# Kernel tuning notes

Measured on AMD Instinct MI355X. Metric: run time of the kernel, lower is better.

Reference implementation:

```python
import jax, jax.numpy as jnp
import numpy as np

N_LAYERS, H, D, DFF, V = 6, 16, 1024, 4096, 512
B, S = 4, 2048
DK = D // H
EPS = 1e-6
NEG = -1000000000.0


def _pe_table(max_len, d):
    pos = np.arange(max_len, dtype=np.float32)[:, None]
    div = 1.0 / (10000.0 ** (np.arange(0, d, 2, dtype=np.float32) / d))
    pe = np.zeros((max_len, d), dtype=np.float32)
    pe[:, 0::2] = np.sin(pos * div)
    pe[:, 1::2] = np.cos(pos * div)
    return jnp.asarray(pe[None])  # [1, max_len, d]


def setup_inputs() -> dict:
    key = jax.random.key(0)
    ks = jax.random.split(key, 20)
    f = lambda k, shp: (jax.random.normal(k, shp, dtype=jnp.float32) * 0.02)
    inp = {
        "tgt": jax.random.randint(ks[0], (B, S), 0, V, dtype=jnp.int64),
        "tgt_mask": jnp.tril(jnp.ones((S, S), dtype=jnp.int32))[None],  # [1,S,S] causal
        "emb": f(ks[1], (V, D)),
        "pe": _pe_table(S, D),
        "Wq": f(ks[2], (N_LAYERS, H, D, DK)), "bq": f(ks[3], (N_LAYERS, H, DK)),
        "Wk": f(ks[4], (N_LAYERS, H, D, DK)), "bk": f(ks[5], (N_LAYERS, H, DK)),
        "Wv": f(ks[6], (N_LAYERS, H, D, DK)), "bv": f(ks[7], (N_LAYERS, H, DK)),
        "Wo": f(ks[8], (N_LAYERS, D, D)), "bo": f(ks[9], (N_LAYERS, D)),
        "W1": f(ks[10], (N_LAYERS, D, DFF)), "b1": f(ks[11], (N_LAYERS, DFF)),
        "W2": f(ks[12], (N_LAYERS, DFF, D)), "b2": f(ks[13], (N_LAYERS, D)),
        "ln1_a": jnp.ones((N_LAYERS, D)), "ln1_b": jnp.zeros((N_LAYERS, D)),
        "ln2_a": jnp.ones((N_LAYERS, D)), "ln2_b": jnp.zeros((N_LAYERS, D)),
        "lnf_a": jnp.ones((D,)), "lnf_b": jnp.zeros((D,)),
    }
    return inp


def _ln(x, a, b):
    # torch: a*(x-mean)/(std+eps)+b with unbiased std
    m = x.mean(-1, keepdims=True)
    var = ((x - m) ** 2).sum(-1, keepdims=True) / (x.shape[-1] - 1)
    return a * (x - m) / (jnp.sqrt(var) + EPS) + b


def reference(tgt, tgt_mask, emb, pe, Wq, bq, Wk, bk, Wv, bv, Wo, bo,
              W1, b1, W2, b2, ln1_a, ln1_b, ln2_a, ln2_b, lnf_a, lnf_b):
    d = emb.shape[1]
    s = tgt.shape[1]
    x = emb[tgt] * jnp.sqrt(jnp.float32(d)) + pe[:, :s]  # [B,S,D]
    dk = Wq.shape[-1]
    scale = jnp.sqrt(jnp.float32(dk))

    def layer(x, p):
        wq, bq_, wk, bk_, wv, bv_, wo, bo_, w1, b1_, w2, b2_, a1, g1, a2, g2 = p
        h = _ln(x, a1, g1)
        q = jnp.einsum('bsd,hdk->bhsk', h, wq) + bq_[:, None, :]
        k = jnp.einsum('bsd,hdk->bhsk', h, wk) + bk_[:, None, :]
        v = jnp.einsum('bsd,hdk->bhsk', h, wv) + bv_[:, None, :]
        sc = jnp.einsum('bhsk,bhtk->bhst', q, k) / scale
        sc = jnp.where(tgt_mask[:, None] == 0, jnp.float32(NEG), sc)
        att = jax.nn.softmax(sc, axis=-1)
        o = jnp.einsum('bhst,bhtk->bhsk', att, v)
        o = o.transpose(0, 2, 1, 3).reshape(x.shape)  # concat heads (head order)
        x = x + (o @ wo + bo_)
        h2 = _ln(x, a2, g2)
        x = x + (jnp.maximum(h2 @ w1 + b1_, 0.0) @ w2 + b2_)
        return x, None

    x, _ = jax.lax.scan(layer, x, (Wq, bq, Wk, bk, Wv, bv, Wo, bo,
                                   W1, b1, W2, b2, ln1_a, ln1_b, ln2_a, ln2_b))
    return _ln(x, lnf_a, lnf_b)
```

## Files before the change

### kernel.cpp

```cpp
#include <hip/hip_runtime.h>

typedef __bf16 bf16;
typedef float f32x4 __attribute__((ext_vector_type(4)));
typedef __bf16 bf16x8 __attribute__((ext_vector_type(8)));
typedef __bf16 bf16x4 __attribute__((ext_vector_type(4)));
typedef __bf16 bf16x2 __attribute__((ext_vector_type(2)));

#define NL 6
#define NH 16
#define DM 1024
#define DFF 4096
#define SEQ 2048
#define NB 4
#define NTOK (NB*SEQ)

__device__ __forceinline__ void gload16(const void* g, void* l) {
  __builtin_amdgcn_global_load_lds((const __attribute__((address_space(1))) void*)g,
                                   (__attribute__((address_space(3))) void*)l, 16, 0, 0);
}

__global__ __launch_bounds__(256) void repack_t(const float* __restrict__ src,
                                                bf16* __restrict__ out, int K, int N) {
  const int l = blockIdx.z;
  const int d0 = blockIdx.x * 32, n0 = blockIdx.y * 32;
  __shared__ float t[32][33];
  const int tx = threadIdx.x & 31, ty = threadIdx.x >> 5;
  const float* s = src + (size_t)l * K * N;
  #pragma unroll
  for (int j = 0; j < 4; ++j)
    t[ty*4 + j][tx] = s[(size_t)(d0 + ty*4 + j) * N + n0 + tx];
  __syncthreads();
  bf16* o = out + (size_t)l * N * K;
  #pragma unroll
  for (int j = 0; j < 4; ++j)
    o[(size_t)(n0 + ty*4 + j) * K + d0 + tx] = (bf16)t[tx][ty*4 + j];
}

__global__ __launch_bounds__(256) void repack_qkv(const float* __restrict__ Wq,
                                                  const float* __restrict__ Wk,
                                                  const float* __restrict__ Wv,
                                                  bf16* __restrict__ out) {
  const int l = blockIdx.z;
  const int d0 = blockIdx.x * 32, n0 = blockIdx.y * 32;
  __shared__ float t[32][33];
  const int tx = threadIdx.x & 31, ty = threadIdx.x >> 5;
  const int which = n0 >> 10, h = (n0 & 1023) >> 6, kh0 = n0 & 63;
  const float* W = (which == 0) ? Wq : (which == 1 ? Wk : Wv);
  const float* s = W + ((size_t)(l*NH + h) * DM) * 64 + kh0;
  #pragma unroll
  for (int j = 0; j < 4; ++j)
    t[ty*4 + j][tx] = s[(size_t)(d0 + ty*4 + j) * 64 + tx];
  __syncthreads();
  bf16* o = out + (size_t)l * 3072 * DM + (size_t)n0 * DM + d0;
  #pragma unroll
  for (int j = 0; j < 4; ++j)
    o[(size_t)(ty*4 + j) * DM + tx] = (bf16)t[tx][ty*4 + j];
}

__global__ __launch_bounds__(256) void repack_b(const float* __restrict__ bq,
                                                const float* __restrict__ bk,
                                                const float* __restrict__ bv,
                                                float* __restrict__ out) {
  const int i = blockIdx.x * 256 + threadIdx.x;
  if (i >= NL * 3072) return;
  const int l = i / 3072, n = i % 3072;
  const int which = n >> 10, h = (n >> 6) & 15, kh = n & 63;
  const float* b = (which == 0) ? bq : (which == 1 ? bk : bv);
  out[i] = b[(l*NH + h) * 64 + kh];
}

__global__ __launch_bounds__(256) void embed_k(const int* __restrict__ tgt,
                                               const float* __restrict__ emb,
                                               const float* __restrict__ pe,
                                               float* __restrict__ x) {
  const int i = blockIdx.x;
  const int spos = i & (SEQ - 1);
  const int tok = tgt[i];
  const int tid = threadIdx.x;
  float4 e = ((const float4*)(emb + (size_t)tok * DM))[tid];
  float4 p = ((const float4*)(pe + (size_t)spos * DM))[tid];
  float4 r; r.x = e.x*32.f + p.x; r.y = e.y*32.f + p.y; r.z = e.z*32.f + p.z; r.w = e.w*32.f + p.w;
  ((float4*)(x + (size_t)i * DM))[tid] = r;
}

template<bool OB>
__global__ __launch_bounds__(256) void ln_k(const float* __restrict__ x,
                                            const float* __restrict__ a,
                                            const float* __restrict__ bsh,
                                            bf16* __restrict__ ob, float* __restrict__ of) {
  __shared__ float red[8];
  const int row = blockIdx.x, tid = threadIdx.x;
  const float4 v = ((const float4*)(x + (size_t)row * DM))[tid];
  float s = v.x + v.y + v.z + v.w;
  #pragma unroll
  for (int off = 32; off > 0; off >>= 1) s += __shfl_down(s, off);
  if ((tid & 63) == 0) red[tid >> 6] = s;
  __syncthreads();
  const float mean = (red[0] + red[1] + red[2] + red[3]) * (1.f / 1024.f);
  const float d0 = v.x - mean, d1 = v.y - mean, d2 = v.z - mean, d3 = v.w - mean;
  float ss = d0*d0 + d1*d1 + d2*d2 + d3*d3;
  #pragma unroll
  for (int off = 32; off > 0; off >>= 1) ss += __shfl_down(ss, off);
  if ((tid & 63) == 0) red[4 + (tid >> 6)] = ss;
  __syncthreads();
  const float var = (red[4] + red[5] + red[6] + red[7]) * (1.f / 1023.f);
  const float inv = 1.f / (sqrtf(var) + 1e-6f);
  const float4 av = ((const float4*)a)[tid];
  const float4 bv = ((const float4*)bsh)[tid];
  const float r0 = av.x * d0 * inv + bv.x;
  const float r1 = av.y * d1 * inv + bv.y;
  const float r2 = av.z * d2 * inv + bv.z;
  const float r3 = av.w * d3 * inv + bv.w;
  if (OB) {
    bf16x4 w; w[0] = (bf16)r0; w[1] = (bf16)r1; w[2] = (bf16)r2; w[3] = (bf16)r3;
    ((bf16x4*)(ob + (size_t)row * DM))[tid] = w;
  } else {
    float4 w; w.x = r0; w.y = r1; w.z = r2; w.w = r3;
    ((float4*)(of + (size_t)row * DM))[tid] = w;
  }
}

#define BARRIER() asm volatile("s_barrier" ::: "memory")
#define VMW(n)    asm volatile("s_waitcnt vmcnt(" #n ")" ::: "memory")

template<int EPI>
__global__ __launch_bounds__(512, 1) void gemm8(const bf16* __restrict__ A,
                                                const bf16* __restrict__ B,
                                                const float* __restrict__ bias,
                                                float* __restrict__ xres,
                                                bf16* __restrict__ outb,
                                                bf16* __restrict__ vtb,
                                                int K, int ldc) {
  constexpr bool SW = (EPI == 1) || (EPI == 2);
  __shared__ __align__(16) char lds[131072];
  const int tid = threadIdx.x;
  const int m0 = blockIdx.x * 256, n0 = blockIdx.y * 256;
  const int wid = tid >> 6, lane = tid & 63;
  const int wm = wid >> 2, wn = wid & 3;
  const int fr = lane & 15, fq = lane >> 4;
  const int fl16 = (fq * 16 + fr) * 16;
  const int s0 = tid, s1 = tid + 512;
  const int r0 = ((s0 >> 7) << 4) | (s0 & 15), c0 = (((s0 >> 6) & 1) << 2) | ((s0 >> 4) & 3);
  const int r1 = ((s1 >> 7) << 4) | (s1 & 15), c1 = (((s1 >> 6) & 1) << 2) | ((s1 >> 4) & 3);
  const bf16* Ap0 = A + (size_t)(m0 + r0) * K + c0 * 8;
  const bf16* Ap1 = A + (size_t)(m0 + r1) * K + c1 * 8;
  const bf16* Bp0 = B + (size_t)(n0 + r0) * K + c0 * 8;
  const bf16* Bp1 = B + (size_t)(n0 + r1) * K + c1 * 8;
  const size_t rskip = (size_t)128 * K;
  const int aRd = wm * 16384;
  const int bRd = 32768 + (wn >> 1) * 16384;
  const int bN = (wn & 1) * 4;

  f32x4 acc[8][4] = {};
  bf16x8 af8[8][2], bfr[4][2];

#define ST_A(d, h, kt) { \
  gload16(Ap0 + (size_t)(h) * rskip + (kt), lds + (d)*65536 + (h)*16384 + s0*16); \
  gload16(Ap1 + (size_t)(h) * rskip + (kt), lds + (d)*65536 + (h)*16384 + s1*16); }
#define ST_B(d, h, kt) { \
  gload16(Bp0 + (size_t)(h) * rskip + (kt), lds + (d)*65536 + 32768 + (h)*16384 + s0*16); \
  gload16(Bp1 + (size_t)(h) * rskip + (kt), lds + (d)*65536 + 32768 + (h)*16384 + s1*16); }
#define LD_A(d, mb) { _Pragma("unroll") for (int m_ = 0; m_ < 4; ++m_) \
    _Pragma("unroll") for (int ks_ = 0; ks_ < 2; ++ks_) \
      af8[(mb) + m_][ks_] = *(const bf16x8*)(lds + (d)*65536 + aRd + ((mb) + m_)*2048 + ks_*1024 + fl16); }
#define LD_B(d, nb) { _Pragma("unroll") for (int n_ = 0; n_ < 2; ++n_) \
    _Pragma("unroll") for (int ks_ = 0; ks_ < 2; ++ks_) \
      bfr[(nb) + n_][ks_] = *(const bf16x8*)(lds + (d)*65536 + bRd + (bN + (nb) + n_)*2048 + ks_*1024 + fl16); }
#define MFMA_Q(mb, nb) { __builtin_amdgcn_s_setprio(1); \
  _Pragma("unroll") for (int m_ = 0; m_ < 4; ++m_) \
  _Pragma("unroll") for (int n_ = 0; n_ < 2; ++n_) \
  _Pragma("unroll") for (int ks_ = 0; ks_ < 2; ++ks_) \
    acc[(mb) + m_][(nb) + n_] = SW ? \
      __builtin_amdgcn_mfma_f32_16x16x32_bf16( \
        bfr[(nb) + n_][ks_], af8[(mb) + m_][ks_], acc[(mb) + m_][(nb) + n_], 0, 0, 0) : \
      __builtin_amdgcn_mfma_f32_16x16x32_bf16( \
        af8[(mb) + m_][ks_], bfr[(nb) + n_][ks_], acc[(mb) + m_][(nb) + n_], 0, 0, 0); \
  __builtin_amdgcn_s_setprio(0); }

  ST_A(0, 0, 0); ST_A(0, 1, 0);
  ST_B(0, 0, 0); ST_B(0, 1, 0);
  ST_A(1, 0, 64); ST_A(1, 1, 64);
  VMW(4);
  BARRIER();

  const int niter = K >> 7;
  for (int it = 0; it < niter; ++it) {
    const int ktB1 = (2 * it + 1) << 6;
    const int ktE2 = (2 * it + 2) << 6;
    const int ktO3 = (2 * it + 3) << 6;
    const bool more = (it + 1 < niter);
    LD_A(0, 0); LD_B(0, 0);
    ST_B(1, 0, ktB1);
    BARRIER(); MFMA_Q(0, 0); BARRIER();
    LD_A(0, 4);
    ST_B(1, 1, ktB1);
    BARRIER(); MFMA_Q(4, 0); BARRIER();
    LD_B(0, 2);
    if (more) ST_A(0, 0, ktE2);
    BARRIER(); MFMA_Q(4, 2); BARRIER();
    if (more) { ST_A(0, 1, ktE2); VMW(4); } else { VMW(0); }
    BARRIER(); MFMA_Q(0, 2); BARRIER();
    LD_A(1, 0); LD_B(1, 0);
    if (more) ST_B(0, 0, ktE2);
    BARRIER(); MFMA_Q(0, 0); BARRIER();
    LD_A(1, 4);
    if (more) ST_B(0, 1, ktE2);
    BARRIER(); MFMA_Q(4, 0); BARRIER();
    LD_B(1, 2);
    if (more) ST_A(1, 0, ktO3);
    BARRIER(); MFMA_Q(4, 2); BARRIER();
    if (more) { ST_A(1, 1, ktO3); VMW(4); }
    BARRIER(); MFMA_Q(0, 2); BARRIER();
  }
#undef ST_A
#undef ST_B
#undef LD_A
#undef LD_B
#undef MFMA_Q

  #pragma unroll
  for (int m = 0; m < 8; ++m) {
    #pragma unroll
    for (int n = 0; n < 4; ++n) {
      if constexpr (SW) {
        const int row = m0 + wm * 128 + m * 16 + fr;
        const int colb = n0 + wn * 64 + n * 16 + fq * 4;
        const float4 b4 = *(const float4*)(bias + colb);
        if constexpr (EPI == 2) {
          bf16x4 w;
          w[0] = (bf16)fmaxf(acc[m][n][0] + b4.x, 0.f);
          w[1] = (bf16)fmaxf(acc[m][n][1] + b4.y, 0.f);
          w[2] = (bf16)fmaxf(acc[m][n][2] + b4.z, 0.f);
          w[3] = (bf16)fmaxf(acc[m][n][3] + b4.w, 0.f);
          *(bf16x4*)(outb + (size_t)row * ldc + colb) = w;
        } else {
          float4* p = (float4*)(xres + (size_t)row * ldc + colb);
          float4 c = *p;
          c.x += acc[m][n][0] + b4.x;
          c.y += acc[m][n][1] + b4.y;
          c.z += acc[m][n][2] + b4.z;
          c.w += acc[m][n][3] + b4.w;
          *p = c;
        }
      } else {
        const int row = m0 + wm * 128 + m * 16 + fq * 4;
        const int col = n0 + wn * 64 + n * 16 + fr;
        const float bc = bias[col];
        #pragma unroll
        for (int j = 0; j < 4; ++j) {
          const float v = acc[m][n][j] + bc;
          outb[(size_t)(row + j) * ldc + col] = (bf16)v;
        }
      }
    }
  }
}

template<int EPI>
__global__ __launch_bounds__(512, 1) void gemm8n(const bf16* __restrict__ A,
                                                 const bf16* __restrict__ B,
                                                 const float* __restrict__ bias,
                                                 float* __restrict__ xres,
                                                 bf16* __restrict__ outb,
                                                 bf16* __restrict__ vtb,
                                                 int K, int ldc) {
  constexpr bool SW = (EPI == 1) || (EPI == 2);
  __shared__ __align__(16) char lds[131072];
  const int tid = threadIdx.x;
  const int m0 = blockIdx.x * 128, n0 = blockIdx.y * 256;
  const int wid = tid >> 6, lane = tid & 63;
  const int wm = wid >> 2, wn = wid & 3;
  const int fr = lane & 15, fq = lane >> 4;
  const int fl16 = (fq * 16 + fr) * 16;
  const int s0 = tid, s1 = tid + 512;
  const int r0 = ((s0 >> 7) << 4) | (s0 & 15), c0 = (((s0 >> 6) & 1) << 2) | ((s0 >> 4) & 3);
  const int r1 = ((s1 >> 7) << 4) | (s1 & 15), c1 = (((s1 >> 6) & 1) << 2) | ((s1 >> 4) & 3);
  const bf16* Ap0 = A + (size_t)(m0 + r0) * K + c0 * 8;
  const bf16* Ap1 = A + (size_t)(m0 + r1) * K + c1 * 8;
  const bf16* Bp0 = B + (size_t)(n0 + r0) * K + c0 * 8;
  const bf16* Bp1 = B + (size_t)(n0 + r1) * K + c1 * 8;
  const size_t rskipB = (size_t)128 * K;
  const int aRd = wm * 8192;
  const int bRd = wn * 8192;

  f32x4 acc[4][4] = {};
  bf16x8 af[4][2], bfr[4][2];

#define ST_An(d, kt) { \
  gload16(Ap0 + (kt), lds + (d)*16384 + s0*16); \
  gload16(Ap1 + (kt), lds + (d)*16384 + s1*16); }
#define ST_Bn(j, h, kt) { \
  gload16(Bp0 + (size_t)(h) * rskipB + (kt), lds + 32768 + (j)*32768 + (h)*16384 + s0*16); \
  gload16(Bp1 + (size_t)(h) * rskipB + (kt), lds + 32768 + (j)*32768 + (h)*16384 + s1*16); }
#define LD_An(d) { _Pragma("unroll") for (int m_ = 0; m_ < 4; ++m_) \
    _Pragma("unroll") for (int ks_ = 0; ks_ < 2; ++ks_) \
      af[m_][ks_] = *(const bf16x8*)(lds + (d)*16384 + aRd + m_*2048 + ks_*1024 + fl16); }
#define LD_Bn(j, nb) { _Pragma("unroll") for (int n_ = 0; n_ < 2; ++n_) \
    _Pragma("unroll") for (int ks_ = 0; ks_ < 2; ++ks_) \
      bfr[(nb) + n_][ks_] = *(const bf16x8*)(lds + 32768 + (j)*32768 + bRd + ((nb) + n_)*2048 + ks_*1024 + fl16); }
#define MFMA_H(nb) { __builtin_amdgcn_s_setprio(1); \
  _Pragma("unroll") for (int m_ = 0; m_ < 4; ++m_) \
  _Pragma("unroll") for (int n_ = 0; n_ < 2; ++n_) \
  _Pragma("unroll") for (int ks_ = 0; ks_ < 2; ++ks_) \
    acc[m_][(nb) + n_] = SW ? \
      __builtin_amdgcn_mfma_f32_16x16x32_bf16( \
        bfr[(nb) + n_][ks_], af[m_][ks_], acc[m_][(nb) + n_], 0, 0, 0) : \
      __builtin_amdgcn_mfma_f32_16x16x32_bf16( \
        af[m_][ks_], bfr[(nb) + n_][ks_], acc[m_][(nb) + n_], 0, 0, 0); \
  __builtin_amdgcn_s_setprio(0); }

  ST_An(0, 0);
  ST_Bn(0, 0, 0); ST_Bn(0, 1, 0);
  ST_An(1, 64);
  ST_Bn(1, 0, 64); ST_Bn(1, 1, 64);
  VMW(0);
  BARRIER();

  const int nt = K >> 6;
  int j = 0;
  for (int t = 0; t < nt; ++t) {
    const int d = t & 1;
    const int j2 = (j + 2 >= 3) ? (j - 1) : (j + 2);
    const bool more = (t + 2 < nt);
    const int kt2 = (t + 2) << 6;
    LD_An(d); LD_Bn(j, 0);
    if (more) { ST_Bn(j2, 0, kt2); ST_Bn(j2, 1, kt2); }
    BARRIER(); MFMA_H(0); BARRIER();
    LD_Bn(j, 2);
    if (more) { ST_An(d, kt2); VMW(6); } else { VMW(0); }
    BARRIER(); MFMA_H(2); BARRIER();
    j = (j + 1 >= 3) ? 0 : (j + 1);
  }
#undef ST_An
#undef ST_Bn
#undef LD_An
#undef LD_Bn
#undef MFMA_H

  #pragma unroll
  for (int m = 0; m < 4; ++m) {
    #pragma unroll
    for (int n = 0; n < 4; ++n) {
      if constexpr (SW) {
        const int row = m0 + wm * 64 + m * 16 + fr;
        const int colb = n0 + wn * 64 + n * 16 + fq * 4;
        const float4 b4 = *(const float4*)(bias + colb);
        if constexpr (EPI == 2) {
          bf16x4 w;
          w[0] = (bf16)fmaxf(acc[m][n][0] + b4.x, 0.f);
          w[1] = (bf16)fmaxf(acc[m][n][1] + b4.y, 0.f);
          w[2] = (bf16)fmaxf(acc[m][n][2] + b4.z, 0.f);
          w[3] = (bf16)fmaxf(acc[m][n][3] + b4.w, 0.f);
          *(bf16x4*)(outb + (size_t)row * ldc + colb) = w;
        } else {
          float4* p = (float4*)(xres + (size_t)row * ldc + colb);
          float4 c = *p;
          c.x += acc[m][n][0] + b4.x;
          c.y += acc[m][n][1] + b4.y;
          c.z += acc[m][n][2] + b4.z;
          c.w += acc[m][n][3] + b4.w;
          *p = c;
        }
      } else {
        const int row = m0 + wm * 64 + m * 16 + fq * 4;
        const int col = n0 + wn * 64 + n * 16 + fr;
        const float bc = bias[col];
        if constexpr (EPI == 3) {
          if (col >= 2048) {
            const int hh = (col - 2048) >> 6, dkk = col & 63;
            const int bb = row >> 11, tt = row & 2047;
            bf16x4 w;
            #pragma unroll
            for (int jj = 0; jj < 4; ++jj) w[jj] = (bf16)(acc[m][n][jj] + bc);
            *(bf16x4*)(vtb + ((((size_t)bb*NH + hh)*64 + dkk)*SEQ + tt)) = w;
            continue;
          }
        }
        #pragma unroll
        for (int jj = 0; jj < 4; ++jj) {
          float v = acc[m][n][jj] + bc;
          if constexpr (EPI == 3) {
            if (col < 1024) v *= 0.125f;
          }
          outb[(size_t)(row + jj) * ldc + col] = (bf16)v;
        }
      }
    }
  }
}

__global__ __launch_bounds__(256) void attn5_k(const bf16* __restrict__ qk,
                                               const bf16* __restrict__ vt,
                                               bf16* __restrict__ o) {
  __shared__ __align__(16) bf16 Ks[2][64 * 64];
  __shared__ __align__(16) bf16 Vs[2][64 * 64];
  __shared__ __align__(16) bf16 Ps[4][16 * 64];
  const int flat = blockIdx.y * 16 + blockIdx.x;
  const int xcd = flat & 7, slot = flat >> 3;
  const int bh = xcd * 8 + (slot >> 4);
  const int pairi = slot & 15;
  const int b = bh >> 4, h = bh & 15;
  const int tid = threadIdx.x;
  const int wave = tid >> 6, lane = tid & 63;
  const int fr = lane & 15, fq = lane >> 4;
  const bf16* Qg = qk + (size_t)b * SEQ * 2048 + h * 64;
  const bf16* Kg = Qg + 1024;
  const bf16* Vtg = vt + (size_t)bh * 64 * SEQ;
  char* Pw = (char*)&Ps[wave][0];
  const int fr7 = fr & 7;

  const int sl0 = tid, sl1 = tid + 256;
  const int sr0 = sl0 >> 3, sm0 = sl0 & 7, sg0 = (sm0 ^ (sr0 & 7)) * 8;
  const int sr1 = sl1 >> 3, sm1 = sl1 & 7, sg1 = (sm1 ^ (sr1 & 7)) * 8;

#define STAGE_KV(db, t0_) { \
    gload16(Kg + (size_t)((t0_) + sr0) * 2048 + sg0, (char*)Ks + (db)*8192 + sl0*16); \
    gload16(Vtg + (size_t)sr0 * SEQ + (t0_) + sg0,   (char*)Vs + (db)*8192 + sl0*16); \
    gload16(Kg + (size_t)((t0_) + sr1) * 2048 + sg1, (char*)Ks + (db)*8192 + sl1*16); \
    gload16(Vtg + (size_t)sr1 * SEQ + (t0_) + sg1,   (char*)Vs + (db)*8192 + sl1*16); }

#define COMPUTE(q0w_, qrow_, qf0_, qf1_, oacc_, lrun_) { \
      f32x4 s_[4] = {}; \
      _Pragma("unroll") \
      for (int n = 0; n < 4; ++n) { \
        const int t_ = n * 16 + fr; \
        const bf16x8 k0 = *(const bf16x8*)(Ksc + (t_ * 8 + (fq ^ (t_ & 7))) * 16); \
        const bf16x8 k1 = *(const bf16x8*)(Ksc + (t_ * 8 + ((fq + 4) ^ (t_ & 7))) * 16); \
        s_[n] = __builtin_amdgcn_mfma_f32_16x16x32_bf16(k0, (qf0_), s_[n], 0, 0, 0); \
        s_[n] = __builtin_amdgcn_mfma_f32_16x16x32_bf16(k1, (qf1_), s_[n], 0, 0, 0); \
      } \
      float sv[16]; \
      _Pragma("unroll") \
      for (int n = 0; n < 4; ++n) \
        _Pragma("unroll") \
        for (int jj = 0; jj < 4; ++jj) \
          sv[n * 4 + jj] = s_[n][jj]; \
      if (t0 + 63 > (q0w_)) { \
        _Pragma("unroll") \
        for (int i = 0; i < 16; ++i) { \
          const int t_abs = t0 + (i >> 2) * 16 + fq * 4 + (i & 3); \
          if (t_abs > (qrow_)) sv[i] = -1e30f; \
        } \
      } \
      _Pragma("unroll") \
      for (int i = 0; i < 16; ++i) sv[i] = __expf(sv[i]); \
      float a8[8]; \
      _Pragma("unroll") \
      for (int i = 0; i < 8; ++i) a8[i] = sv[i] + sv[i + 8]; \
      float a4[4]; \
      _Pragma("unroll") \
      for (int i = 0; i < 4; ++i) a4[i] = a8[i] + a8[i + 4]; \
      float ps = (a4[0] + a4[1]) + (a4[2] + a4[3]); \
      ps += __shfl_xor(ps, 16); \
      ps += __shfl_xor(ps, 32); \
      (lrun_) += ps; \
      _Pragma("unroll") \
      for (int n = 0; n < 4; ++n) \
        _Pragma("unroll") \
        for (int jp = 0; jp < 2; ++jp) { \
          bf16x2 w; w[0] = (bf16)sv[n * 4 + jp * 2]; w[1] = (bf16)sv[n * 4 + jp * 2 + 1]; \
          const int byteoff = n * 32 + fq * 8 + jp * 4; \
          const int chunk = byteoff >> 4, within = byteoff & 15; \
          *(bf16x2*)(Pw + fr * 128 + ((chunk ^ fr7) << 4) + within) = w; \
        } \
      _Pragma("unroll") \
      for (int ks = 0; ks < 2; ++ks) { \
        const bf16x8 pa = *(const bf16x8*)(Pw + fr * 128 + (((ks * 4 + fq) ^ fr7) << 4)); \
        _Pragma("unroll") \
        for (int nd = 0; nd < 4; ++nd) { \
          const int dk_ = nd * 16 + fr; \
          const bf16x8 vf = *(const bf16x8*)(Vsc + (dk_ * 8 + ((ks * 4 + fq) ^ (dk_ & 7))) * 16); \
          (oacc_)[nd] = __builtin_amdgcn_mfma_f32_16x16x32_bf16(pa, vf, (oacc_)[nd], 0, 0, 0); \
        } \
      } }

  const int qbA = pairi;
  const int qbB = 31 - pairi;
  const int q0A = qbA * 64 + wave * 16, q0B = qbB * 64 + wave * 16;
  const int qrA = q0A + fr, qrB = q0B + fr;
  const bf16x8 qA0 = *(const bf16x8*)(Qg + (size_t)qrA * 2048 + fq * 8);
  const bf16x8 qA1 = *(const bf16x8*)(Qg + (size_t)qrA * 2048 + 32 + fq * 8);
  const bf16x8 qB0 = *(const bf16x8*)(Qg + (size_t)qrB * 2048 + fq * 8);
  const bf16x8 qB1 = *(const bf16x8*)(Qg + (size_t)qrB * 2048 + 32 + fq * 8);
  f32x4 oaccA[4] = {}, oaccB[4] = {};
  float lA = 0.f, lB = 0.f;
  const int nt = qbB + 1;

  STAGE_KV(0, 0);
  for (int kt = 0; kt < nt; ++kt) {
    const int t0 = kt * 64;
    const int db = kt & 1;
    __syncthreads();
    if (kt + 1 < nt) {
      STAGE_KV(db ^ 1, (kt + 1) * 64);
      VMW(4);
    } else {
      VMW(0);
    }
    __syncthreads();
    const char* Ksc = (char*)Ks + db * 8192;
    const char* Vsc = (char*)Vs + db * 8192;
    if (t0 <= q0A + 15) COMPUTE(q0A, qrA, qA0, qA1, oaccA, lA);
    COMPUTE(q0B, qrB, qB0, qB1, oaccB, lB);
  }
#undef COMPUTE
#undef STAGE_KV

  {
    float lv[4];
    #pragma unroll
    for (int jj = 0; jj < 4; ++jj) lv[jj] = __shfl(lA, fq * 4 + jj);
    #pragma unroll
    for (int nd = 0; nd < 4; ++nd) {
      const int col = h * 64 + nd * 16 + fr;
      #pragma unroll
      for (int jj = 0; jj < 4; ++jj) {
        const int row = q0A + fq * 4 + jj;
        o[((size_t)b * SEQ + row) * DM + col] = (bf16)(oaccA[nd][jj] / lv[jj]);
      }
    }
    #pragma unroll
    for (int jj = 0; jj < 4; ++jj) lv[jj] = __shfl(lB, fq * 4 + jj);
    #pragma unroll
    for (int nd = 0; nd < 4; ++nd) {
      const int col = h * 64 + nd * 16 + fr;
      #pragma unroll
      for (int jj = 0; jj < 4; ++jj) {
        const int row = q0B + fq * 4 + jj;
        o[((size_t)b * SEQ + row) * DM + col] = (bf16)(oaccB[nd][jj] / lv[jj]);
      }
    }
  }
}

extern "C" void kernel_launch(void* const* d_in, const int* in_sizes, int n_in,
                              void* d_out, int out_size, void* d_ws, size_t ws_size,
                              hipStream_t stream) {
  const int*   tgt  = (const int*)d_in[0];
  const float* emb  = (const float*)d_in[2];
  const float* pe   = (const float*)d_in[3];
  const float* Wq   = (const float*)d_in[4];
  const float* bq   = (const float*)d_in[5];
  const float* Wk   = (const float*)d_in[6];
  const float* bk   = (const float*)d_in[7];
  const float* Wv   = (const float*)d_in[8];
  const float* bv   = (const float*)d_in[9];
  const float* Wo   = (const float*)d_in[10];
  const float* bo   = (const float*)d_in[11];
  const float* W1   = (const float*)d_in[12];
  const float* b1   = (const float*)d_in[13];
  const float* W2   = (const float*)d_in[14];
  const float* b2   = (const float*)d_in[15];
  const float* ln1a = (const float*)d_in[16];
  const float* ln1b = (const float*)d_in[17];
  const float* ln2a = (const float*)d_in[18];
  const float* ln2b = (const float*)d_in[19];
  const float* lnfa = (const float*)d_in[20];
  const float* lnfb = (const float*)d_in[21];

  char* ws = (char*)d_ws;
  size_t off = 0;
  bf16*  wqkv = (bf16*)(ws + off);  off += (size_t)NL * 3072 * DM * 2;
  bf16*  wo_  = (bf16*)(ws + off);  off += (size_t)NL * DM * DM * 2;
  bf16*  w1_  = (bf16*)(ws + off);  off += (size_t)NL * DFF * DM * 2;
  bf16*  w2_  = (bf16*)(ws + off);  off += (size_t)NL * DM * DFF * 2;
  float* bqkv = (float*)(ws + off); off += (size_t)NL * 3072 * 4;
  float* x    = (float*)(ws + off); off += (size_t)NTOK * DM * 4;
  bf16*  hbuf = (bf16*)(ws + off);  off += (size_t)NTOK * DM * 2;
  bf16*  qkb  = (bf16*)(ws + off);  off += (size_t)NTOK * 2048 * 2;
  bf16*  vtb  = (bf16*)(ws + off);  off += (size_t)NB * NH * 64 * SEQ * 2;
  bf16*  obuf = (bf16*)(ws + off);  off += (size_t)NTOK * DM * 2;
  bf16*  ubuf = qkb;

  repack_qkv<<<dim3(32, 96, NL), 256, 0, stream>>>(Wq, Wk, Wv, wqkv);
  repack_t  <<<dim3(32, 32, NL), 256, 0, stream>>>(Wo, wo_, DM, DM);
  repack_t  <<<dim3(32, 128, NL), 256, 0, stream>>>(W1, w1_, DM, DFF);
  repack_t  <<<dim3(128, 32, NL), 256, 0, stream>>>(W2, w2_, DFF, DM);
  repack_b  <<<72, 256, 0, stream>>>(bq, bk, bv, bqkv);
  embed_k   <<<NTOK, 256, 0, stream>>>(tgt, emb, pe, x);

  for (int l = 0; l < NL; ++l) {
    ln_k<true><<<NTOK, 256, 0, stream>>>(x, ln1a + l * DM, ln1b + l * DM, hbuf, nullptr);
    gemm8n<3><<<dim3(64, 12), 512, 0, stream>>>(hbuf, wqkv + (size_t)l * 3072 * DM,
                                                bqkv + l * 3072, nullptr, qkb, vtb, DM, 2048);
    attn5_k<<<dim3(16, 64), 256, 0, stream>>>(qkb, vtb, obuf);
    gemm8n<1><<<dim3(64, 4), 512, 0, stream>>>(obuf, wo_ + (size_t)l * DM * DM,
                                               bo + l * DM, x, nullptr, nullptr, DM, DM);
    ln_k<true><<<NTOK, 256, 0, stream>>>(x, ln2a + l * DM, ln2b + l * DM, hbuf, nullptr);
    gemm8<2><<<dim3(32, 16), 512, 0, stream>>>(hbuf, w1_ + (size_t)l * DFF * DM,
                                               b1 + l * DFF, nullptr, ubuf, nullptr, DM, DFF);
    gemm8n<1><<<dim3(64, 4), 512, 0, stream>>>(ubuf, w2_ + (size_t)l * DM * DFF,
                                               b2 + l * DM, x, nullptr, nullptr, DFF, DM);
  }
  ln_k<false><<<NTOK, 256, 0, stream>>>(x, lnfa, lnfb, nullptr, (float*)d_out);

  (void)in_sizes; (void)n_in; (void)out_size; (void)ws_size;
}
```

Baseline: 2.612 ms.

## Switch QKV projection to gemm8 with V-transpose epilogue, add attention MFMA priority

The QKV projection now runs on the gemm8 kernel (bigger tiles, fewer blocks), and a new EPI==3 path in gemm8's epilogue writes V transposed straight into vtb and scales Q by 1/8. The attention kernel raises wave priority around its MFMA sections with s_setprio, and the final normalisation uses a reciprocal multiply instead of a divide. The aim is better reuse in the QKV GEMM and better MFMA issue in attention. The risk is that the gemm8 EPI==3 path may not match gemm8n's Q scaling and V layout, and the larger tiles give a grid of only 384 blocks.

```diff
diff --git a/kernel.cpp b/kernel.cpp
--- a/kernel.cpp
+++ b/kernel.cpp
@@ -246,9 +246,23 @@
         const int row = m0 + wm * 128 + m * 16 + fq * 4;
         const int col = n0 + wn * 64 + n * 16 + fr;
         const float bc = bias[col];
+        if constexpr (EPI == 3) {
+          if (col >= 2048) {
+            const int hh = (col - 2048) >> 6, dkk = col & 63;
+            const int bb = row >> 11, tt = row & 2047;
+            bf16x4 w;
+            #pragma unroll
+            for (int jj = 0; jj < 4; ++jj) w[jj] = (bf16)(acc[m][n][jj] + bc);
+            *(bf16x4*)(vtb + ((((size_t)bb*NH + hh)*64 + dkk)*SEQ + tt)) = w;
+            continue;
+          }
+        }
         #pragma unroll
         for (int j = 0; j < 4; ++j) {
-          const float v = acc[m][n][j] + bc;
+          float v = acc[m][n][j] + bc;
+          if constexpr (EPI == 3) {
+            if (col < 1024) v *= 0.125f;
+          }
           outb[(size_t)(row + j) * ldc + col] = (bf16)v;
         }
       }
@@ -421,6 +435,7 @@
 
 #define COMPUTE(q0w_, qrow_, qf0_, qf1_, oacc_, lrun_) { \
       f32x4 s_[4] = {}; \
+      __builtin_amdgcn_s_setprio(1); \
       _Pragma("unroll") \
       for (int n = 0; n < 4; ++n) { \
         const int t_ = n * 16 + fr; \
@@ -429,6 +444,7 @@
         s_[n] = __builtin_amdgcn_mfma_f32_16x16x32_bf16(k0, (qf0_), s_[n], 0, 0, 0); \
         s_[n] = __builtin_amdgcn_mfma_f32_16x16x32_bf16(k1, (qf1_), s_[n], 0, 0, 0); \
       } \
+      __builtin_amdgcn_s_setprio(0); \
       float sv[16]; \
       _Pragma("unroll") \
       for (int n = 0; n < 4; ++n) \
@@ -463,6 +479,7 @@
           const int chunk = byteoff >> 4, within = byteoff & 15; \
           *(bf16x2*)(Pw + fr * 128 + ((chunk ^ fr7) << 4) + within) = w; \
         } \
+      __builtin_amdgcn_s_setprio(1); \
       _Pragma("unroll") \
       for (int ks = 0; ks < 2; ++ks) { \
         const bf16x8 pa = *(const bf16x8*)(Pw + fr * 128 + (((ks * 4 + fq) ^ fr7) << 4)); \
@@ -472,7 +489,8 @@
           const bf16x8 vf = *(const bf16x8*)(Vsc + (dk_ * 8 + ((ks * 4 + fq) ^ (dk_ & 7))) * 16); \
           (oacc_)[nd] = __builtin_amdgcn_mfma_f32_16x16x32_bf16(pa, vf, (oacc_)[nd], 0, 0, 0); \
         } \
-      } }
+      } \
+      __builtin_amdgcn_s_setprio(0); }
 
   const int qbA = pairi;
   const int qbB = 31 - pairi;
@@ -507,27 +525,27 @@
 #undef STAGE_KV
 
   {
-    float lv[4];
+    float li[4];
     #pragma unroll
-    for (int jj = 0; jj < 4; ++jj) lv[jj] = __shfl(lA, fq * 4 + jj);
+    for (int jj = 0; jj < 4; ++jj) li[jj] = 1.f / __shfl(lA, fq * 4 + jj);
     #pragma unroll
     for (int nd = 0; nd < 4; ++nd) {
       const int col = h * 64 + nd * 16 + fr;
       #pragma unroll
       for (int jj = 0; jj < 4; ++jj) {
         const int row = q0A + fq * 4 + jj;
-        o[((size_t)b * SEQ + row) * DM + col] = (bf16)(oaccA[nd][jj] / lv[jj]);
+        o[((size_t)b * SEQ + row) * DM + col] = (bf16)(oaccA[nd][jj] * li[jj]);
       }
     }
     #pragma unroll
-    for (int jj = 0; jj < 4; ++jj) lv[jj] = __shfl(lB, fq * 4 + jj);
+    for (int jj = 0; jj < 4; ++jj) li[jj] = 1.f / __shfl(lB, fq * 4 + jj);
     #pragma unroll
     for (int nd = 0; nd < 4; ++nd) {
       const int col = h * 64 + nd * 16 + fr;
       #pragma unroll
       for (int jj = 0; jj < 4; ++jj) {
         const int row = q0B + fq * 4 + jj;
-        o[((size_t)b * SEQ + row) * DM + col] = (bf16)(oaccB[nd][jj] / lv[jj]);
+        o[((size_t)b * SEQ + row) * DM + col] = (bf16)(oaccB[nd][jj] * li[jj]);
       }
     }
   }
@@ -581,8 +599,8 @@
 
   for (int l = 0; l < NL; ++l) {
     ln_k<true><<<NTOK, 256, 0, stream>>>(x, ln1a + l * DM, ln1b + l * DM, hbuf, nullptr);
-    gemm8n<3><<<dim3(64, 12), 512, 0, stream>>>(hbuf, wqkv + (size_t)l * 3072 * DM,
-                                                bqkv + l * 3072, nullptr, qkb, vtb, DM, 2048);
+    gemm8<3><<<dim3(32, 12), 512, 0, stream>>>(hbuf, wqkv + (size_t)l * 3072 * DM,
+                                               bqkv + l * 3072, nullptr, qkb, vtb, DM, 2048);
     attn5_k<<<dim3(16, 64), 256, 0, stream>>>(qkb, vtb, obuf);
     gemm8n<1><<<dim3(64, 4), 512, 0, stream>>>(obuf, wo_ + (size_t)l * DM * DM,
                                                bo + l * DM, x, nullptr, nullptr, DM, DM);
```

Measured after the change: 2.548 ms. 2.5% less time.
